# Kernel optimization log

Measured on AMD Instinct MI355X. Metric: run time of the kernel, lower is better.

## Reference

```python
import jax, jax.numpy as jnp
import numpy as np

DIM = 3072
NUM_HEADS = 24
HEAD_DIM = DIM // NUM_HEADS  # 128
EPS = 1e-6


def rms_norm(x, scale):
    # x: (..., D); torch F.rms_norm over last dim
    var = jnp.mean(jnp.square(x), axis=-1, keepdims=True)
    return x * jax.lax.rsqrt(var + EPS) * scale


def apply_rope(xq, xk, freqs_cis):
    # xq, xk: (B, H, L, D); freqs_cis: (1, 1, L, D//2, 2, 2)
    B, H, L, D = xq.shape
    xq_ = xq.astype(jnp.float32).reshape(B, H, L, D // 2, 1, 2)
    xk_ = xk.astype(jnp.float32).reshape(B, H, L, D // 2, 1, 2)
    # (1,1,L,D/2,2) * (B,H,L,D/2,1) broadcast -> (B,H,L,D/2,2)
    xq_out = freqs_cis[..., 0] * xq_[..., 0] + freqs_cis[..., 1] * xq_[..., 1]
    xk_out = freqs_cis[..., 0] * xk_[..., 0] + freqs_cis[..., 1] * xk_[..., 1]
    return xq_out.reshape(B, H, L, D).astype(xq.dtype), xk_out.reshape(B, H, L, D).astype(xk.dtype)


def setup_inputs() -> dict:
    key = jax.random.key(0)
    ks = jax.random.split(key, 7)
    B, L = 1, 2048
    x = jax.random.normal(ks[0], (B, L, DIM), dtype=jnp.float32)
    pe = jax.random.normal(ks[1], (1, 1, L, HEAD_DIM // 2, 2, 2), dtype=jnp.float32)
    # parameters (torch nn.Linear layout: weight is (out, in))
    s = 1.0 / np.sqrt(DIM)
    w_qkv = jax.random.uniform(ks[2], (3 * DIM, DIM), minval=-s, maxval=s, dtype=jnp.float32)
    w_proj = jax.random.uniform(ks[3], (DIM, DIM), minval=-s, maxval=s, dtype=jnp.float32)
    b_proj = jax.random.uniform(ks[4], (DIM,), minval=-s, maxval=s, dtype=jnp.float32)
    q_scale = jnp.ones((HEAD_DIM,), dtype=jnp.float32)
    k_scale = jnp.ones((HEAD_DIM,), dtype=jnp.float32)
    return {"x": x, "pe": pe, "w_qkv": w_qkv, "w_proj": w_proj,
            "b_proj": b_proj, "q_scale": q_scale, "k_scale": k_scale}


def reference(x, pe, w_qkv, w_proj, b_proj, q_scale, k_scale):
    B, L, _ = x.shape
    qkv = x @ w_qkv.T  # (B, L, 3*DIM)
    qkv = qkv.reshape(B, L, 3, NUM_HEADS, HEAD_DIM)
    qkv = jnp.transpose(qkv, (2, 0, 3, 1, 4))  # (3, B, H, L, D)
    q, k, v = qkv[0], qkv[1], qkv[2]
    # QKNorm (RMSNorm over head_dim)
    q = rms_norm(q, q_scale)
    k = rms_norm(k, k_scale)
    # RoPE
    q, k = apply_rope(q, k, pe)
    # SDPA: softmax(q k^T / sqrt(D)) v, non-causal
    scores = jnp.einsum("bhqd,bhkd->bhqk", q, k) / np.sqrt(HEAD_DIM).astype(np.float32)
    attn = jax.nn.softmax(scores, axis=-1)
    out = jnp.einsum("bhqk,bhkd->bhqd", attn, v)  # (B, H, L, D)
    out = jnp.transpose(out, (0, 2, 1, 3)).reshape(B, L, DIM)  # B L (H D)
    return out @ w_proj.T + b_proj
```

## Files before the change

kernel.cpp:

```cpp
#include <hip/hip_runtime.h>
#include <hip/hip_bf16.h>

typedef _Float16 f16;
typedef _Float16 f16x2 __attribute__((ext_vector_type(2)));
typedef _Float16 f16x4 __attribute__((ext_vector_type(4)));
typedef _Float16 f16x8 __attribute__((ext_vector_type(8)));
typedef float f32x4 __attribute__((ext_vector_type(4)));

#define L_SEQ 2048
#define DIM 3072
#define NHEAD 24
#define HDIM 128

__device__ __forceinline__ void gll16(const f16* g, f16* l) {
    __builtin_amdgcn_global_load_lds((const __attribute__((address_space(1))) void*)g,
                                     (__attribute__((address_space(3))) void*)l, 16, 0, 0);
}

__global__ __launch_bounds__(256) void cvt3_kernel(const float* __restrict__ s0, f16* __restrict__ d0, int n0,
                                                   const float* __restrict__ s1, f16* __restrict__ d1, int n1,
                                                   const float* __restrict__ s2, f16* __restrict__ d2, int n2) {
    int i = blockIdx.x * blockDim.x + threadIdx.x;
    int stride = gridDim.x * blockDim.x;
    for (int j = i; j < n0; j += stride) {
        float4 v = reinterpret_cast<const float4*>(s0)[j];
        f16x4 o = {(f16)v.x, (f16)v.y, (f16)v.z, (f16)v.w};
        reinterpret_cast<f16x4*>(d0)[j] = o;
    }
    for (int j = i; j < n1; j += stride) {
        float4 v = reinterpret_cast<const float4*>(s1)[j];
        f16x4 o = {(f16)v.x, (f16)v.y, (f16)v.z, (f16)v.w};
        reinterpret_cast<f16x4*>(d1)[j] = o;
    }
    for (int j = i; j < n2; j += stride) {
        float4 v = reinterpret_cast<const float4*>(s2)[j];
        f16x4 o = {(f16)v.x, (f16)v.y, (f16)v.z, (f16)v.w};
        reinterpret_cast<f16x4*>(d2)[j] = o;
    }
}


#define GEMM_BODY_S(T, VM, DO_STAGE)                                                    \
    {                                                                                   \
        asm volatile("s_waitcnt vmcnt(" #VM ")" ::: "memory");                          \
        __builtin_amdgcn_s_barrier();                                                   \
        __builtin_amdgcn_sched_barrier(0);                                              \
        const int slot_ = (T) % 3;                                                      \
        f16x8 af[4], bf[4];                                                             \
        _Pragma("unroll") for (int i = 0; i < 4; i++)                                   \
            af[i] = *reinterpret_cast<const f16x8*>(                                    \
                &As[slot_][(wr + i * 16 + laneM) * 32 + fc16]);                         \
        _Pragma("unroll") for (int j = 0; j < 4; j++)                                   \
            bf[j] = *reinterpret_cast<const f16x8*>(                                    \
                &Bs[slot_][(wc + j * 16 + laneM) * 32 + fc16]);                         \
        if (DO_STAGE) {                                                                 \
            const int t2 = (T) + 2;                                                     \
            const int s2 = t2 % 3;                                                      \
            gll16(Asrc + t2 * 32, &As[s2][dstoff]);                                     \
            gll16(Asrc + (size_t)64 * K + t2 * 32, &As[s2][2048 + dstoff]);             \
            gll16(Bsrc + t2 * 32, &Bs[s2][dstoff]);                                     \
            gll16(Bsrc + (size_t)64 * K + t2 * 32, &Bs[s2][2048 + dstoff]);             \
        }                                                                               \
        __builtin_amdgcn_s_setprio(1);                                                  \
        _Pragma("unroll") for (int i = 0; i < 4; i++)                                   \
            _Pragma("unroll") for (int j = 0; j < 4; j++)                               \
                acc[i][j] =                                                             \
                    __builtin_amdgcn_mfma_f32_16x16x32_f16(af[i], bf[j], acc[i][j],     \
                                                           0, 0, 0);                    \
        __builtin_amdgcn_s_setprio(0);                                                  \
    }

template <int MODE>
__global__ __launch_bounds__(256, 4) void rg128_gemm(const f16* __restrict__ A,
                                                     const f16* __restrict__ B,
                                                     f16* __restrict__ Cf16,
                                                     f16* __restrict__ vT,
                                                     float* __restrict__ Cf32,
                                                     const float* __restrict__ bias,
                                                     int M, int N, int K) {
    __shared__ f16 As[3][128 * 32];
    __shared__ f16 Bs[3][128 * 32];
    const int tid = threadIdx.x;
    const int wid = tid >> 6;
    const int lane = tid & 63;
    const int grp = lane >> 4;
    const int laneM = lane & 15;

    const int nwg = gridDim.x * gridDim.y;
    const int orig = blockIdx.y * gridDim.x + blockIdx.x;
    const int wgid = (orig & 7) * (nwg >> 3) + (orig >> 3);
    const int by = wgid % gridDim.y;
    const int bx = wgid / gridDim.y;
    const int m0 = by * 128;
    const int n0 = bx * 128;

    const int wr = (wid >> 1) * 64;
    const int wc = (wid & 1) * 64;
    const int NT = K >> 5;
    const int fc16 = (grp ^ ((laneM >> 1) & 3)) * 8;

    const int srow = tid >> 2;
    const int scol = (((tid & 3) ^ ((tid >> 3) & 3)) << 3);
    const f16* Asrc = A + (size_t)(m0 + srow) * K + scol;
    const f16* Bsrc = B + (size_t)(n0 + srow) * K + scol;
    const int dstoff = wid * 512;

    const f32x4 vzero = {0.f, 0.f, 0.f, 0.f};
    f32x4 acc[4][4];
#pragma unroll
    for (int i = 0; i < 4; i++)
#pragma unroll
        for (int j = 0; j < 4; j++) acc[i][j] = vzero;

#pragma unroll
    for (int t = 0; t < 2; t++) {
        gll16(Asrc + t * 32, &As[t][dstoff]);
        gll16(Asrc + (size_t)64 * K + t * 32, &As[t][2048 + dstoff]);
        gll16(Bsrc + t * 32, &Bs[t][dstoff]);
        gll16(Bsrc + (size_t)64 * K + t * 32, &Bs[t][2048 + dstoff]);
    }

    int t = 0;
    for (; t < NT - 2; ++t) GEMM_BODY_S(t, 4, true);
    GEMM_BODY_S(t, 4, false); ++t;
    GEMM_BODY_S(t, 0, false);

    if (MODE == 1) {
#pragma unroll
        for (int i = 0; i < 4; i++)
#pragma unroll
            for (int j = 0; j < 4; j++)
#pragma unroll
                for (int r = 0; r < 4; r++) {
                    int row = m0 + wr + i * 16 + grp * 4 + r;
                    int col = n0 + wc + j * 16 + laneM;
                    Cf32[(size_t)row * N + col] = acc[i][j][r] + bias[col];
                }
    } else if (n0 < 2 * DIM) {
#pragma unroll
        for (int i = 0; i < 4; i++)
#pragma unroll
            for (int j = 0; j < 4; j++)
#pragma unroll
                for (int r = 0; r < 4; r++) {
                    int row = m0 + wr + i * 16 + grp * 4 + r;
                    int col = n0 + wc + j * 16 + laneM;
                    Cf16[(size_t)row * N + col] = (f16)acc[i][j][r];
                }
    } else {
#pragma unroll
        for (int i = 0; i < 4; i++)
#pragma unroll
            for (int j = 0; j < 4; j++) {
                int hd = n0 - 2 * DIM + wc + j * 16 + laneM;
                int row0 = m0 + wr + i * 16 + grp * 4;
                f16x4 pk;
#pragma unroll
                for (int r = 0; r < 4; r++) pk[r] = (f16)acc[i][j][r];
                *reinterpret_cast<f16x4*>(&vT[(size_t)hd * L_SEQ + row0]) = pk;
            }
    }
}

__global__ __launch_bounds__(256) void fuse_qk_kernel(const f16* __restrict__ qkv,
                                                      const float* __restrict__ pe,
                                                      const float* __restrict__ qs,
                                                      const float* __restrict__ ks,
                                                      f16* __restrict__ qb,
                                                      f16* __restrict__ kb) {
    const int l = blockIdx.x;
    const int h = blockIdx.y * 4 + (threadIdx.x >> 6);
    const int i = threadIdx.x & 63;
    const f16* row = qkv + (size_t)l * (3 * DIM) + h * HDIM;
    f16x2 qp = *reinterpret_cast<const f16x2*>(row + 2 * i);
    f16x2 kp = *reinterpret_cast<const f16x2*>(row + DIM + 2 * i);
    float q0 = (float)qp[0], q1 = (float)qp[1];
    float k0 = (float)kp[0], k1 = (float)kp[1];
    float sq = q0 * q0 + q1 * q1;
    float sk = k0 * k0 + k1 * k1;
#pragma unroll
    for (int off = 1; off < 64; off <<= 1) {
        sq += __shfl_xor(sq, off);
        sk += __shfl_xor(sk, off);
    }
    const float SCALE = 0.08838834764831845f;
    float rq = rsqrtf(sq * (1.0f / 128.0f) + 1e-6f) * SCALE;
    float rk = rsqrtf(sk * (1.0f / 128.0f) + 1e-6f);
    float4 w = *reinterpret_cast<const float4*>(pe + ((size_t)l * 64 + i) * 4);
    float qa = q0 * rq * qs[2 * i];
    float qbv = q1 * rq * qs[2 * i + 1];
    float ka = k0 * rk * ks[2 * i];
    float kbv = k1 * rk * ks[2 * i + 1];
    f16x2 qo = {(f16)(w.x * qa + w.y * qbv), (f16)(w.z * qa + w.w * qbv)};
    f16x2 ko = {(f16)(w.x * ka + w.y * kbv), (f16)(w.z * ka + w.w * kbv)};
    *reinterpret_cast<f16x2*>(qb + ((size_t)h * L_SEQ + l) * HDIM + 2 * i) = qo;
    *reinterpret_cast<f16x2*>(kb + ((size_t)h * L_SEQ + l) * HDIM + 2 * i) = ko;
}

#define KVBLK 64
#define NSTEP (L_SEQ / KVBLK)

__device__ __forceinline__ void stage_kv(const f16* __restrict__ Kh,
                                         const f16* __restrict__ Vh,
                                         int k0, f16* Kt, f16* Vt, int tid) {
    const int wid = tid >> 6;
    const int krow = tid >> 4;
    const int kcl = (tid & 15) ^ (krow & 7);
    const int vrow = tid >> 3;
    const int vcl = (tid & 7) ^ (vrow & 7);
#pragma unroll
    for (int i = 0; i < 4; i++)
        gll16(Kh + (size_t)(k0 + i * 16 + krow) * HDIM + kcl * 8, Kt + i * 2048 + wid * 512);
#pragma unroll
    for (int i = 0; i < 4; i++)
        gll16(Vh + (size_t)(i * 32 + vrow) * L_SEQ + k0 + vcl * 8, Vt + i * 2048 + wid * 512);
}

__global__ __launch_bounds__(256, 2) void attn_kernel(const f16* __restrict__ qb,
                                                      const f16* __restrict__ kb,
                                                      const f16* __restrict__ vT,
                                                      f16* __restrict__ attnb) {
    __shared__ f16 Kt[2][64 * 128];
    __shared__ f16 Vt[2][128 * 64];
    __shared__ f16 Pl[4][16 * 72];
    const int tid = threadIdx.x;
    const int wid = tid >> 6;
    const int lane = tid & 63;
    const int grp = lane >> 4;
    const int laneM = lane & 15;

    const int nwg = gridDim.x * gridDim.y;
    const int orig = blockIdx.y * gridDim.x + blockIdx.x;
    const int wgid = (orig & 7) * (nwg >> 3) + (orig >> 3);
    const int h = wgid / gridDim.x;
    const int q0 = (wgid % gridDim.x) * 64 + wid * 16;

    const f16* Qh = qb + (size_t)h * L_SEQ * HDIM;
    const f16* Kh = kb + (size_t)h * L_SEQ * HDIM;
    const f16* Vh = vT + (size_t)h * HDIM * L_SEQ;

    f16x8 qf[4];
#pragma unroll
    for (int c = 0; c < 4; c++)
        qf[c] = *reinterpret_cast<const f16x8*>(Qh + (size_t)(q0 + laneM) * HDIM + c * 32 + grp * 8);

    const f32x4 vzero = {0.f, 0.f, 0.f, 0.f};
    f32x4 O[8];
#pragma unroll
    for (int f = 0; f < 8; f++) O[f] = vzero;
    float m = -3.0e38f;
    float lsum = 0.f;
    f16* Prow = &Pl[wid][laneM * 72];
    const int swz = laneM & 7;

    stage_kv(Kh, Vh, 0, Kt[0], Vt[0], tid);

    for (int step = 0; step < NSTEP; ++step) {
        const int cur = step & 1;
        __syncthreads();
        if (step + 1 < NSTEP)
            stage_kv(Kh, Vh, (step + 1) * KVBLK, Kt[cur ^ 1], Vt[cur ^ 1], tid);
        const f16* Kc = Kt[cur];
        const f16* Vc = Vt[cur];

        f32x4 s[4];
#pragma unroll
        for (int cc = 0; cc < 4; cc++) s[cc] = vzero;
#pragma unroll
        for (int cc = 0; cc < 4; cc++) {
            f16x8 kf[4];
#pragma unroll
            for (int c = 0; c < 4; c++)
                kf[c] = *reinterpret_cast<const f16x8*>(
                    &Kc[(cc * 16 + laneM) * 128 + (((c * 4 + grp) ^ swz) * 8)]);
#pragma unroll
            for (int c = 0; c < 4; c++)
                s[cc] = __builtin_amdgcn_mfma_f32_16x16x32_f16(kf[c], qf[c], s[cc], 0, 0, 0);
        }

        float pmax = s[0][0];
#pragma unroll
        for (int cc = 0; cc < 4; cc++)
#pragma unroll
            for (int r = 0; r < 4; r++) pmax = fmaxf(pmax, s[cc][r]);
        if (!__all(pmax <= m + 8.0f)) {
            float pm = fmaxf(pmax, __shfl_xor(pmax, 16));
            pm = fmaxf(pm, __shfl_xor(pm, 32));
            float mnew = fmaxf(m, pm);
            float alpha = __expf(m - mnew);
            m = mnew;
            lsum *= alpha;
            float af[4];
#pragma unroll
            for (int r = 0; r < 4; r++) af[r] = __shfl(alpha, grp * 4 + r);
#pragma unroll
            for (int f = 0; f < 8; f++)
#pragma unroll
                for (int r = 0; r < 4; r++) O[f][r] *= af[r];
        }
        float ps = 0.f;
#pragma unroll
        for (int cc = 0; cc < 4; cc++) {
            f16x4 pk;
#pragma unroll
            for (int r = 0; r < 4; r++) {
                float p = __expf(s[cc][r] - m);
                ps += p;
                pk[r] = (f16)p;
            }
            *reinterpret_cast<f16x4*>(Prow + cc * 16 + grp * 4) = pk;
        }
        ps += __shfl_xor(ps, 16);
        ps += __shfl_xor(ps, 32);
        lsum += ps;

#pragma unroll
        for (int z = 0; z < 2; z++) {
            f16x8 pa = *reinterpret_cast<const f16x8*>(Prow + z * 32 + grp * 8);
#pragma unroll
            for (int f = 0; f < 8; f++) {
                f16x8 vf = *reinterpret_cast<const f16x8*>(
                    &Vc[(f * 16 + laneM) * 64 + (((z * 4 + grp) ^ swz) * 8)]);
                O[f] = __builtin_amdgcn_mfma_f32_16x16x32_f16(pa, vf, O[f], 0, 0, 0);
            }
        }
    }

    float li = 1.0f / lsum;
    float lf[4];
#pragma unroll
    for (int r = 0; r < 4; r++) lf[r] = __shfl(li, grp * 4 + r);
#pragma unroll
    for (int f = 0; f < 8; f++)
#pragma unroll
        for (int r = 0; r < 4; r++) {
            int row = q0 + grp * 4 + r;
            attnb[(size_t)row * DIM + h * HDIM + f * 16 + laneM] = (f16)(O[f][r] * lf[r]);
        }
}

extern "C" void kernel_launch(void* const* d_in, const int* in_sizes, int n_in,
                              void* d_out, int out_size, void* d_ws, size_t ws_size,
                              hipStream_t stream) {
    const float* x = (const float*)d_in[0];
    const float* pe = (const float*)d_in[1];
    const float* w_qkv = (const float*)d_in[2];
    const float* w_proj = (const float*)d_in[3];
    const float* b_proj = (const float*)d_in[4];
    const float* q_scale = (const float*)d_in[5];
    const float* k_scale = (const float*)d_in[6];
    float* out = (float*)d_out;

    char* ws = (char*)d_ws;
    f16* xb     = (f16*)(ws + 0);
    f16* wqkvb  = (f16*)(ws + 12582912);
    f16* wprojb = (f16*)(ws + 69206016);
    f16* qkvb   = (f16*)(ws + 88080384);
    f16* qbuf   = (f16*)(ws + 125829120);
    f16* kbuf   = (f16*)(ws + 138412032);
    f16* vT     = (f16*)(ws + 150994944);
    f16* attnb  = (f16*)(ws + 163577856);
    if (ws_size < 176160768) return;

    cvt3_kernel<<<2048, 256, 0, stream>>>(x, xb, (2048 * 3072) / 4,
                                          w_qkv, wqkvb, (9216 * 3072) / 4,
                                          w_proj, wprojb, (3072 * 3072) / 4);

    rg128_gemm<0><<<dim3(72, 16), 256, 0, stream>>>(xb, wqkvb, qkvb, vT, nullptr, nullptr,
                                                    2048, 9216, 3072);
    fuse_qk_kernel<<<dim3(2048, 6), 256, 0, stream>>>(qkvb, pe, q_scale, k_scale, qbuf, kbuf);
    attn_kernel<<<dim3(32, 24), 256, 0, stream>>>(qbuf, kbuf, vT, attnb);
    rg128_gemm<1><<<dim3(24, 16), 256, 0, stream>>>(attnb, wprojb, nullptr, nullptr, out, b_proj,
                                                    2048, 3072, 3072);
}
```

Measured before the change: 360.4 us.

## Split-K the output projection GEMM into two halves plus a reduce-bias kernel

Replaces the single output-projection GEMM (384 workgroups) with a split-K version over two K halves (768 workgroups), which writes fp16 partials into reused workspace regions. A separate kernel then sums the partials and adds the bias in fp32. The aim is to fill the device's compute units better with more workgroups. In exchange it adds partial-buffer traffic, an extra launch, and rounds each partial to fp16 before the sum.

```diff
diff --git a/kernel.cpp b/kernel.cpp
--- a/kernel.cpp
+++ b/kernel.cpp
@@ -162,6 +162,95 @@
     }
 }
 
+__global__ __launch_bounds__(256, 4) void proj_sk_gemm(const f16* __restrict__ A,
+                                                       const f16* __restrict__ B,
+                                                       f16* __restrict__ P0,
+                                                       f16* __restrict__ P1,
+                                                       int M, int N, int K) {
+    __shared__ f16 As[3][128 * 32];
+    __shared__ f16 Bs[3][128 * 32];
+    const int tid = threadIdx.x;
+    const int wid = tid >> 6;
+    const int lane = tid & 63;
+    const int grp = lane >> 4;
+    const int laneM = lane & 15;
+
+    const int gxy = gridDim.x * gridDim.y;
+    const int nwg = gxy * gridDim.z;
+    const int orig = (blockIdx.z * gridDim.y + blockIdx.y) * gridDim.x + blockIdx.x;
+    const int wgid = (orig & 7) * (nwg >> 3) + (orig >> 3);
+    const int bz = wgid / gxy;
+    const int rem = wgid % gxy;
+    const int by = rem % gridDim.y;
+    const int bx = rem / gridDim.y;
+    const int m0 = by * 128;
+    const int n0 = bx * 128;
+    const int kbase = bz * 1536;
+    f16* __restrict__ P = bz ? P1 : P0;
+
+    const int wr = (wid >> 1) * 64;
+    const int wc = (wid & 1) * 64;
+    const int NT = 48;
+    const int fc16 = (grp ^ ((laneM >> 1) & 3)) * 8;
+
+    const int srow = tid >> 2;
+    const int scol = (((tid & 3) ^ ((tid >> 3) & 3)) << 3);
+    const f16* Asrc = A + (size_t)(m0 + srow) * K + kbase + scol;
+    const f16* Bsrc = B + (size_t)(n0 + srow) * K + kbase + scol;
+    const int dstoff = wid * 512;
+
+    const f32x4 vzero = {0.f, 0.f, 0.f, 0.f};
+    f32x4 acc[4][4];
+#pragma unroll
+    for (int i = 0; i < 4; i++)
+#pragma unroll
+        for (int j = 0; j < 4; j++) acc[i][j] = vzero;
+
+#pragma unroll
+    for (int t = 0; t < 2; t++) {
+        gll16(Asrc + t * 32, &As[t][dstoff]);
+        gll16(Asrc + (size_t)64 * K + t * 32, &As[t][2048 + dstoff]);
+        gll16(Bsrc + t * 32, &Bs[t][dstoff]);
+        gll16(Bsrc + (size_t)64 * K + t * 32, &Bs[t][2048 + dstoff]);
+    }
+
+    int t = 0;
+    for (; t < NT - 2; ++t) GEMM_BODY_S(t, 4, true);
+    GEMM_BODY_S(t, 4, false); ++t;
+    GEMM_BODY_S(t, 0, false);
+
+#pragma unroll
+    for (int i = 0; i < 4; i++)
+#pragma unroll
+        for (int j = 0; j < 4; j++)
+#pragma unroll
+            for (int r = 0; r < 4; r++) {
+                int row = m0 + wr + i * 16 + grp * 4 + r;
+                int col = n0 + wc + j * 16 + laneM;
+                P[(size_t)row * N + col] = (f16)acc[i][j][r];
+            }
+}
+
+__global__ __launch_bounds__(256) void reduce2_bias_kernel(const f16* __restrict__ p0,
+                                                           const f16* __restrict__ p1,
+                                                           const float* __restrict__ bias,
+                                                           float* __restrict__ out) {
+    const int n4 = L_SEQ * DIM / 4;
+    int i = blockIdx.x * blockDim.x + threadIdx.x;
+    int stride = gridDim.x * blockDim.x;
+    for (; i < n4; i += stride) {
+        f16x4 a = reinterpret_cast<const f16x4*>(p0)[i];
+        f16x4 b = reinterpret_cast<const f16x4*>(p1)[i];
+        float4 d = reinterpret_cast<const float4*>(bias)[i % (DIM / 4)];
+        float4 o;
+        o.x = (float)a[0] + (float)b[0] + d.x;
+        o.y = (float)a[1] + (float)b[1] + d.y;
+        o.z = (float)a[2] + (float)b[2] + d.z;
+        o.w = (float)a[3] + (float)b[3] + d.w;
+        reinterpret_cast<float4*>(out)[i] = o;
+    }
+}
+
 __global__ __launch_bounds__(256) void fuse_qk_kernel(const f16* __restrict__ qkv,
                                                       const float* __restrict__ pe,
                                                       const float* __restrict__ qs,
@@ -360,6 +449,8 @@
     f16* kbuf   = (f16*)(ws + 138412032);
     f16* vT     = (f16*)(ws + 150994944);
     f16* attnb  = (f16*)(ws + 163577856);
+    f16* p0 = (f16*)(ws + 0);
+    f16* p1 = (f16*)(ws + 12582912);
     if (ws_size < 176160768) return;
 
     cvt3_kernel<<<2048, 256, 0, stream>>>(x, xb, (2048 * 3072) / 4,
@@ -370,6 +461,7 @@
                                                     2048, 9216, 3072);
     fuse_qk_kernel<<<dim3(2048, 6), 256, 0, stream>>>(qkvb, pe, q_scale, k_scale, qbuf, kbuf);
     attn_kernel<<<dim3(32, 24), 256, 0, stream>>>(qbuf, kbuf, vT, attnb);
-    rg128_gemm<1><<<dim3(24, 16), 256, 0, stream>>>(attnb, wprojb, nullptr, nullptr, out, b_proj,
-                                                    2048, 3072, 3072);
-}
+    proj_sk_gemm<<<dim3(24, 16, 2), 256, 0, stream>>>(attnb, wprojb, p0, p1,
+                                                      2048, 3072, 3072);
+    reduce2_bias_kernel<<<1024, 256, 0, stream>>>(p0, p1, b_proj, out);
+}
```

Measured after the change: 370.8 us. +2.9%, slower.

## Process two 16-row query groups per wavefront in attention to reuse K/V fragments

Applied to the files above, without the earlier changes.

Each wavefront in the attention kernel now handles 32 query rows as two 16-row groups instead of 16, so each block covers 128 queries and the grid is halved. K fragments loaded from LDS feed MFMAs for both groups, and each staged K/V tile serves twice as many queries, which cuts LDS reads and global K/V traffic per query. The cost is roughly double the accumulator and Q-fragment registers, with some risk of lower occupancy. Fewer blocks also means only 384 workgroups for 256 CUs, which can leave the load across CUs uneven.

```diff
diff --git a/kernel.cpp b/kernel.cpp
--- a/kernel.cpp
+++ b/kernel.cpp
@@ -38,7 +38,6 @@
         reinterpret_cast<f16x4*>(d2)[j] = o;
     }
 }
-
 
 #define GEMM_BODY_S(T, VM, DO_STAGE)                                                    \
     {                                                                                   \
@@ -233,23 +232,28 @@
     const int orig = blockIdx.y * gridDim.x + blockIdx.x;
     const int wgid = (orig & 7) * (nwg >> 3) + (orig >> 3);
     const int h = wgid / gridDim.x;
-    const int q0 = (wgid % gridDim.x) * 64 + wid * 16;
+    const int q0 = (wgid % gridDim.x) * 128 + wid * 32;
 
     const f16* Qh = qb + (size_t)h * L_SEQ * HDIM;
     const f16* Kh = kb + (size_t)h * L_SEQ * HDIM;
     const f16* Vh = vT + (size_t)h * HDIM * L_SEQ;
 
-    f16x8 qf[4];
-#pragma unroll
-    for (int c = 0; c < 4; c++)
-        qf[c] = *reinterpret_cast<const f16x8*>(Qh + (size_t)(q0 + laneM) * HDIM + c * 32 + grp * 8);
+    f16x8 qf[2][4];
+#pragma unroll
+    for (int g = 0; g < 2; g++)
+#pragma unroll
+        for (int c = 0; c < 4; c++)
+            qf[g][c] = *reinterpret_cast<const f16x8*>(
+                Qh + (size_t)(q0 + g * 16 + laneM) * HDIM + c * 32 + grp * 8);
 
     const f32x4 vzero = {0.f, 0.f, 0.f, 0.f};
-    f32x4 O[8];
-#pragma unroll
-    for (int f = 0; f < 8; f++) O[f] = vzero;
-    float m = -3.0e38f;
-    float lsum = 0.f;
+    f32x4 O[2][8];
+#pragma unroll
+    for (int g = 0; g < 2; g++)
+#pragma unroll
+        for (int f = 0; f < 8; f++) O[g][f] = vzero;
+    float m[2] = {-3.0e38f, -3.0e38f};
+    float lsum[2] = {0.f, 0.f};
     f16* Prow = &Pl[wid][laneM * 72];
     const int swz = laneM & 7;
 
@@ -263,9 +267,11 @@
         const f16* Kc = Kt[cur];
         const f16* Vc = Vt[cur];
 
-        f32x4 s[4];
-#pragma unroll
-        for (int cc = 0; cc < 4; cc++) s[cc] = vzero;
+        f32x4 s[2][4];
+#pragma unroll
+        for (int g = 0; g < 2; g++)
+#pragma unroll
+            for (int cc = 0; cc < 4; cc++) s[g][cc] = vzero;
 #pragma unroll
         for (int cc = 0; cc < 4; cc++) {
             f16x8 kf[4];
@@ -274,69 +280,77 @@
                 kf[c] = *reinterpret_cast<const f16x8*>(
                     &Kc[(cc * 16 + laneM) * 128 + (((c * 4 + grp) ^ swz) * 8)]);
 #pragma unroll
-            for (int c = 0; c < 4; c++)
-                s[cc] = __builtin_amdgcn_mfma_f32_16x16x32_f16(kf[c], qf[c], s[cc], 0, 0, 0);
+            for (int c = 0; c < 4; c++) {
+                s[0][cc] = __builtin_amdgcn_mfma_f32_16x16x32_f16(kf[c], qf[0][c], s[0][cc], 0, 0, 0);
+                s[1][cc] = __builtin_amdgcn_mfma_f32_16x16x32_f16(kf[c], qf[1][c], s[1][cc], 0, 0, 0);
+            }
         }
 
-        float pmax = s[0][0];
-#pragma unroll
-        for (int cc = 0; cc < 4; cc++)
-#pragma unroll
-            for (int r = 0; r < 4; r++) pmax = fmaxf(pmax, s[cc][r]);
-        if (!__all(pmax <= m + 8.0f)) {
-            float pm = fmaxf(pmax, __shfl_xor(pmax, 16));
-            pm = fmaxf(pm, __shfl_xor(pm, 32));
-            float mnew = fmaxf(m, pm);
-            float alpha = __expf(m - mnew);
-            m = mnew;
-            lsum *= alpha;
-            float af[4];
-#pragma unroll
-            for (int r = 0; r < 4; r++) af[r] = __shfl(alpha, grp * 4 + r);
-#pragma unroll
-            for (int f = 0; f < 8; f++)
-#pragma unroll
-                for (int r = 0; r < 4; r++) O[f][r] *= af[r];
+#pragma unroll
+        for (int g = 0; g < 2; g++) {
+            float pmax = s[g][0][0];
+#pragma unroll
+            for (int cc = 0; cc < 4; cc++)
+#pragma unroll
+                for (int r = 0; r < 4; r++) pmax = fmaxf(pmax, s[g][cc][r]);
+            if (!__all(pmax <= m[g] + 8.0f)) {
+                float pm = fmaxf(pmax, __shfl_xor(pmax, 16));
+                pm = fmaxf(pm, __shfl_xor(pm, 32));
+                float mnew = fmaxf(m[g], pm);
+                float alpha = __expf(m[g] - mnew);
+                m[g] = mnew;
+                lsum[g] *= alpha;
+                float af[4];
+#pragma unroll
+                for (int r = 0; r < 4; r++) af[r] = __shfl(alpha, grp * 4 + r);
+#pragma unroll
+                for (int f = 0; f < 8; f++)
+#pragma unroll
+                    for (int r = 0; r < 4; r++) O[g][f][r] *= af[r];
+            }
+            float ps = 0.f;
+#pragma unroll
+            for (int cc = 0; cc < 4; cc++) {
+                f16x4 pk;
+#pragma unroll
+                for (int r = 0; r < 4; r++) {
+                    float p = __expf(s[g][cc][r] - m[g]);
+                    ps += p;
+                    pk[r] = (f16)p;
+                }
+                *reinterpret_cast<f16x4*>(Prow + cc * 16 + grp * 4) = pk;
+            }
+            ps += __shfl_xor(ps, 16);
+            ps += __shfl_xor(ps, 32);
+            lsum[g] += ps;
+
+#pragma unroll
+            for (int z = 0; z < 2; z++) {
+                f16x8 pa = *reinterpret_cast<const f16x8*>(Prow + z * 32 + grp * 8);
+#pragma unroll
+                for (int f = 0; f < 8; f++) {
+                    f16x8 vf = *reinterpret_cast<const f16x8*>(
+                        &Vc[(f * 16 + laneM) * 64 + (((z * 4 + grp) ^ swz) * 8)]);
+                    O[g][f] = __builtin_amdgcn_mfma_f32_16x16x32_f16(pa, vf, O[g][f], 0, 0, 0);
+                }
+            }
         }
-        float ps = 0.f;
-#pragma unroll
-        for (int cc = 0; cc < 4; cc++) {
-            f16x4 pk;
+    }
+
+#pragma unroll
+    for (int g = 0; g < 2; g++) {
+        float li = 1.0f / lsum[g];
+        float lf[4];
+#pragma unroll
+        for (int r = 0; r < 4; r++) lf[r] = __shfl(li, grp * 4 + r);
+#pragma unroll
+        for (int f = 0; f < 8; f++)
 #pragma unroll
             for (int r = 0; r < 4; r++) {
-                float p = __expf(s[cc][r] - m);
-                ps += p;
-                pk[r] = (f16)p;
-            }
-            *reinterpret_cast<f16x4*>(Prow + cc * 16 + grp * 4) = pk;
-        }
-        ps += __shfl_xor(ps, 16);
-        ps += __shfl_xor(ps, 32);
-        lsum += ps;
-
-#pragma unroll
-        for (int z = 0; z < 2; z++) {
-            f16x8 pa = *reinterpret_cast<const f16x8*>(Prow + z * 32 + grp * 8);
-#pragma unroll
-            for (int f = 0; f < 8; f++) {
-                f16x8 vf = *reinterpret_cast<const f16x8*>(
-                    &Vc[(f * 16 + laneM) * 64 + (((z * 4 + grp) ^ swz) * 8)]);
-                O[f] = __builtin_amdgcn_mfma_f32_16x16x32_f16(pa, vf, O[f], 0, 0, 0);
-            }
-        }
-    }
-
-    float li = 1.0f / lsum;
-    float lf[4];
-#pragma unroll
-    for (int r = 0; r < 4; r++) lf[r] = __shfl(li, grp * 4 + r);
-#pragma unroll
-    for (int f = 0; f < 8; f++)
-#pragma unroll
-        for (int r = 0; r < 4; r++) {
-            int row = q0 + grp * 4 + r;
-            attnb[(size_t)row * DIM + h * HDIM + f * 16 + laneM] = (f16)(O[f][r] * lf[r]);
-        }
+                int row = q0 + g * 16 + grp * 4 + r;
+                attnb[(size_t)row * DIM + h * HDIM + f * 16 + laneM] = (f16)(O[g][f][r] * lf[r]);
+            }
+    }
 }
 
 extern "C" void kernel_launch(void* const* d_in, const int* in_sizes, int n_in,
@@ -369,7 +383,7 @@
     rg128_gemm<0><<<dim3(72, 16), 256, 0, stream>>>(xb, wqkvb, qkvb, vT, nullptr, nullptr,
                                                     2048, 9216, 3072);
     fuse_qk_kernel<<<dim3(2048, 6), 256, 0, stream>>>(qkvb, pe, q_scale, k_scale, qbuf, kbuf);
-    attn_kernel<<<dim3(32, 24), 256, 0, stream>>>(qbuf, kbuf, vT, attnb);
+    attn_kernel<<<dim3(16, 24), 256, 0, stream>>>(qbuf, kbuf, vT, attnb);
     rg128_gemm<1><<<dim3(24, 16), 256, 0, stream>>>(attnb, wprojb, nullptr, nullptr, out, b_proj,
                                                     2048, 3072, 3072);
 }
```

Measured after the change: 341.3 us (median of 2 runs). -5.3%, faster.
